# Performance work log

Measured on AMD Instinct MI355X. Metric: run time of the kernel, lower is better.

## Reference

```python
import jax, jax.numpy as jnp
import numpy as np

B, DIM, H, W = 2, 64, 128, 128
D_STATE = 8
D_INNER = int(2.0 * DIM)          # 128
DT_RANK = int(np.ceil(DIM / 16))  # 4
CDBL = DT_RANK + 2 * D_STATE      # 20
HID = 3 * DIM                     # 192 (ffn_expansion_factor=3)
PS = 8                            # EDFFN patch size
EPS = 1e-5


def setup_inputs() -> dict:
    key = jax.random.key(0)
    ks = jax.random.split(key, 20)
    n = lambda k, s, sc=0.02: jax.random.normal(k, s, jnp.float32) * sc
    # dt bias init as in SS2D.dt_init
    rng = np.random.default_rng(0)
    dt = np.exp(rng.uniform(size=D_INNER) * (np.log(0.1) - np.log(0.001)) + np.log(0.001)).clip(min=1e-4)
    dt_b = (dt + np.log(-np.expm1(-dt))).astype(np.float32)
    A_logs = np.log(np.arange(1, D_STATE + 1, dtype=np.float32))[None, :].repeat(D_INNER, 0)
    return {
        "x": jax.random.normal(ks[0], (B, DIM, H, W), jnp.float32),
        "norm1_w": jnp.ones((DIM,), jnp.float32), "norm1_b": jnp.zeros((DIM,), jnp.float32),
        "in_proj_w": n(ks[1], (2 * D_INNER, DIM)),
        "conv2d_w": n(ks[2], (D_INNER, 1, 3, 3), 0.1), "conv2d_b": jnp.zeros((D_INNER,), jnp.float32),
        "x_proj_w": n(ks[3], (CDBL, D_INNER)),
        "x_conv_w": n(ks[4], (CDBL, 1, 7), 0.1), "x_conv_b": jnp.zeros((CDBL,), jnp.float32),
        "dt_w": n(ks[5], (D_INNER, DT_RANK), DT_RANK ** -0.5), "dt_b": jnp.asarray(dt_b),
        "A_logs": jnp.asarray(A_logs), "Ds": jnp.ones((D_INNER,), jnp.float32),
        "out_norm_w": jnp.ones((D_INNER,), jnp.float32), "out_norm_b": jnp.zeros((D_INNER,), jnp.float32),
        "out_proj_w": n(ks[6], (DIM, D_INNER)),
        "norm2_w": jnp.ones((DIM,), jnp.float32), "norm2_b": jnp.zeros((DIM,), jnp.float32),
        "pin_w": n(ks[7], (2 * HID, DIM)),
        "dw_w": n(ks[8], (2 * HID, 1, 3, 3), 0.1),
        "fft_param": jnp.ones((DIM, 1, 1, PS, PS // 2 + 1), jnp.float32),
        "pout_w": n(ks[9], (DIM, HID)),
    }


def _ln_ch(x, w, b):  # LayerNorm over channel dim of BCHW (WithBias_LayerNorm)
    mu = x.mean(1, keepdims=True)
    var = x.var(1, keepdims=True)
    return (x - mu) / jnp.sqrt(var + EPS) * w[None, :, None, None] + b[None, :, None, None]


def _dwconv2d(x, w, b=None):
    y = jax.lax.conv_general_dilated(x, w, (1, 1), [(1, 1), (1, 1)],
                                     dimension_numbers=("NCHW", "OIHW", "NCHW"),
                                     feature_group_count=x.shape[1])
    return y if b is None else y + b[None, :, None, None]


def _dwconv1d(x, w, b):
    y = jax.lax.conv_general_dilated(x, w, (1,), [(3, 3)],
                                     dimension_numbers=("NCH", "OIH", "NCH"),
                                     feature_group_count=x.shape[1])
    return y + b[None, :, None]


def _gelu(x):
    return jax.nn.gelu(x, approximate=False)


def _selective_scan(u, delta, A, Bs, Cs, Ds):
    # u, delta: [B,D,L]; A: [D,N]; Bs, Cs: [B,N,L]; Ds: [D]
    dA = jnp.exp(jnp.einsum("bdl,dn->lbdn", delta, A))          # [L,B,D,N]
    dBu = jnp.einsum("bdl,bnl->lbdn", delta * u, Bs)            # [L,B,D,N]
    Cseq = jnp.transpose(Cs, (2, 0, 1))                         # [L,B,N]

    def step(h, inp):
        dA_l, dBu_l, C_l = inp
        h = dA_l * h + dBu_l
        y = jnp.einsum("bdn,bn->bd", h, C_l)
        return h, y

    h0 = jnp.zeros(dA.shape[1:], dA.dtype)
    _, ys = jax.lax.scan(step, h0, (dA, dBu, Cseq))             # ys: [L,B,D]
    y = jnp.transpose(ys, (1, 2, 0))                            # [B,D,L]
    return y + Ds[None, :, None] * u


def _ss2d(x, in_proj_w, conv2d_w, conv2d_b, x_proj_w, x_conv_w, x_conv_b,
          dt_w, dt_b, A_logs, Ds, out_norm_w, out_norm_b, out_proj_w):
    b, c, h, w = x.shape
    xh = jnp.transpose(x, (0, 2, 3, 1))                          # [B,H,W,C]
    xz = jnp.einsum("bhwc,oc->bhwo", xh, in_proj_w)
    xi, z = jnp.split(xz, 2, axis=-1)
    xi = jnp.transpose(xi, (0, 3, 1, 2))                         # [B,Di,H,W]
    xi = _gelu(_dwconv2d(xi, conv2d_w, conv2d_b))
    L = h * w
    xs = xi.reshape(b, D_INNER, L)
    x_dbl = jnp.einsum("bdl,cd->bcl", xs, x_proj_w)
    x_dbl = _dwconv1d(x_dbl, x_conv_w, x_conv_b)
    dts, Bs, Cs = x_dbl[:, :DT_RANK], x_dbl[:, DT_RANK:DT_RANK + D_STATE], x_dbl[:, DT_RANK + D_STATE:]
    dts = jnp.einsum("brl,dr->bdl", dts, dt_w)
    delta = jax.nn.softplus(dts + dt_b[None, :, None])
    A = -jnp.exp(A_logs)
    y = _selective_scan(xs, delta, A, Bs, Cs, Ds)                # [B,Di,L]
    y = jnp.transpose(y, (0, 2, 1)).reshape(b, h, w, D_INNER)
    mu = y.mean(-1, keepdims=True)
    var = y.var(-1, keepdims=True)
    y = (y - mu) / jnp.sqrt(var + EPS) * out_norm_w + out_norm_b
    y = y * _gelu(z)
    out = jnp.einsum("bhwd,cd->bhwc", y, out_proj_w)
    return jnp.transpose(out, (0, 3, 1, 2))


def _edffn(x, pin_w, dw_w, fft_param, pout_w):
    b, c, h, w = x.shape
    y = jnp.einsum("bchw,oc->bohw", x, pin_w)                    # [B,2*HID,H,W]
    y = _dwconv2d(y, dw_w)
    x1, x2 = jnp.split(y, 2, axis=1)
    y = _gelu(x1) * x2
    y = jnp.einsum("bchw,oc->bohw", y, pout_w)                   # [B,DIM,H,W]
    # per-8x8-patch FFT filtering
    p = y.reshape(b, DIM, h // PS, PS, w // PS, PS).transpose(0, 1, 2, 4, 3, 5)
    pf = jnp.fft.rfft2(p, axes=(-2, -1)) * fft_param
    p = jnp.fft.irfft2(pf, s=(PS, PS), axes=(-2, -1))
    return p.transpose(0, 1, 2, 4, 3, 5).reshape(b, DIM, h, w)


def reference(x, norm1_w, norm1_b, in_proj_w, conv2d_w, conv2d_b, x_proj_w, x_conv_w,
              x_conv_b, dt_w, dt_b, A_logs, Ds, out_norm_w, out_norm_b, out_proj_w,
              norm2_w, norm2_b, pin_w, dw_w, fft_param, pout_w):
    # EVS forward, att=True, idx=3 (odd -> flip H,W)
    x = jnp.flip(x, axis=(-2, -1))
    x = x + _ss2d(_ln_ch(x, norm1_w, norm1_b), in_proj_w, conv2d_w, conv2d_b,
                  x_proj_w, x_conv_w, x_conv_b, dt_w, dt_b, A_logs, Ds,
                  out_norm_w, out_norm_b, out_proj_w)
    x = x + _edffn(_ln_ch(x, norm2_w, norm2_b), pin_w, dw_w, fft_param, pout_w)
    return x
```

## Files before the change

### kernel.cpp

```cpp
#include <hip/hip_runtime.h>
#include <hip/hip_bf16.h>

#define DEV __device__ __forceinline__

constexpr int BATCH = 2;
constexpr int DIM   = 64;
constexpr int HH    = 128, WW = 128;
constexpr int L     = HH * WW;
constexpr int DIN   = 128;
constexpr int DST   = 8;
constexpr int CDBL  = 20;
constexpr int HID   = 192;
constexpr int SEG   = 256;
constexpr int NSEG  = L / SEG;
constexpr int NSEGA = 256;

constexpr long OFF_XF    = 0;
constexpr long OFF_T     = OFF_XF    + (long)BATCH*DIM*L;
constexpr long OFF_XZ    = OFF_T     + (long)BATCH*DIM*L;
constexpr long OFF_XS    = OFF_XZ    + (long)BATCH*2*DIN*L;
constexpr long OFF_DBL   = OFF_XS    + (long)BATCH*DIN*L;
constexpr long OFF_DBL2  = OFF_DBL   + (long)BATCH*CDBL*L;
constexpr long OFF_DELTA = OFF_DBL2  + (long)BATCH*CDBL*L;
constexpr long OFF_Y     = OFF_DELTA + (long)BATCH*DIN*L;
constexpr long OFF_HEND  = OFF_Y     + (long)BATCH*DIN*L;
constexpr long OFF_APROD = OFF_HEND  + (long)BATCH*DIN*NSEGA*DST;
constexpr long OFF_CARRY = OFF_APROD + (long)BATCH*DIN*NSEGA*DST;
constexpr long OFF_H1    = OFF_XS;
constexpr long OFF_YFF   = OFF_H1    + (long)BATCH*2*HID*L;
constexpr long OFF_G     = OFF_CARRY;
constexpr long OFF_AEXP  = OFF_DELTA;

DEV float gelu_f(float x) { return 0.5f * x * (1.0f + erff(x * 0.70710678118654752f)); }
DEV float softplus_f(float x) { return fmaxf(x, 0.f) + log1pf(__expf(-fabsf(x))); }

template<bool FLIPSAVE>
__global__ void ln_ch_k(const float* __restrict__ in, const float* __restrict__ w,
                        const float* __restrict__ bvec, float* __restrict__ outn,
                        float* __restrict__ src_out) {
    int l = blockIdx.x * 256 + threadIdx.x;
    int b = blockIdx.y;
    long base = (long)b * DIM * L;
    int sl = FLIPSAVE ? (L - 1 - l) : l;
    float v[DIM];
    float mu = 0.f;
    #pragma unroll
    for (int c = 0; c < DIM; c++) { v[c] = in[base + (long)c * L + sl]; mu += v[c]; }
    mu *= (1.f / DIM);
    float var = 0.f;
    #pragma unroll
    for (int c = 0; c < DIM; c++) { float d = v[c] - mu; var += d * d; }
    var *= (1.f / DIM);
    float rs = rsqrtf(var + 1e-5f);
    #pragma unroll
    for (int c = 0; c < DIM; c++) {
        long o = base + (long)c * L + l;
        if (FLIPSAVE) src_out[o] = v[c];
        outn[o] = (v[c] - mu) * rs * w[c] + bvec[c];
    }
}

template<int N, int K, int NT, int PIX, int ACT>
__global__ void gemm4(const float* __restrict__ in, long in_bs,
                      const float* __restrict__ Wm,
                      float* __restrict__ out, long out_bs,
                      const float* __restrict__ aux, long aux_bs) {
    static_assert(N % NT == 0, "NT");
    int l = (blockIdx.x * 256 + threadIdx.x) * PIX;
    int b = blockIdx.y;
    int n0 = blockIdx.z * NT;
    const float* Ap = in + (long)b * in_bs + l;
    float acc[NT][PIX];
    #pragma unroll
    for (int i = 0; i < NT; i++)
        #pragma unroll
        for (int p = 0; p < PIX; p++) acc[i][p] = 0.f;
    #pragma unroll 4
    for (int k = 0; k < K; k++) {
        float a[PIX];
        if (PIX == 4) {
            float4 a4 = *(const float4*)(Ap + (long)k * L);
            a[0] = a4.x; a[1] = a4.y; a[2] = a4.z; a[3] = a4.w;
        } else if (PIX == 2) {
            float2 a2 = *(const float2*)(Ap + (long)k * L);
            a[0] = a2.x; a[1] = a2.y;
        } else {
            a[0] = Ap[(long)k * L];
        }
        #pragma unroll
        for (int i = 0; i < NT; i++) {
            float wv = Wm[(long)(n0 + i) * K + k];
            #pragma unroll
            for (int p = 0; p < PIX; p++) acc[i][p] = fmaf(a[p], wv, acc[i][p]);
        }
    }
    #pragma unroll
    for (int i = 0; i < NT; i++) {
        long pos = (long)b * out_bs + (long)(n0 + i) * L + l;
        float r[PIX];
        #pragma unroll
        for (int p = 0; p < PIX; p++) r[p] = acc[i][p];
        if (ACT == 2) {
            const float* rp = aux + (long)b * aux_bs + (long)(n0 + i) * L + l;
            #pragma unroll
            for (int p = 0; p < PIX; p++) r[p] += rp[p];
        }
        if (PIX == 4) {
            float4 st = {r[0], r[1], r[2], r[3]};
            *(float4*)(out + pos) = st;
        } else if (PIX == 2) {
            float2 st = {r[0], r[1]};
            *(float2*)(out + pos) = st;
        } else {
            out[pos] = r[0];
        }
    }
}

__global__ void dwconv3x3_bias_gelu(const float* __restrict__ in, long in_bs,
                                    const float* __restrict__ wgt, const float* __restrict__ bias,
                                    float* __restrict__ out, long out_bs) {
    int l4 = (blockIdx.x * 256 + threadIdx.x) * 4;
    int c = blockIdx.y, b = blockIdx.z;
    int h = l4 >> 7, w = l4 & 127;
    const float* ip = in + (long)b * in_bs + (long)c * L;
    float wv[9];
    #pragma unroll
    for (int i = 0; i < 9; i++) wv[i] = wgt[c * 9 + i];
    float bz = bias[c];
    float acc[4] = {bz, bz, bz, bz};
    #pragma unroll
    for (int kh = 0; kh < 3; kh++) {
        int hh = h + kh - 1;
        if (hh < 0 || hh >= HH) continue;
        const float* row = ip + hh * WW + w;
        float4 m = *(const float4*)row;
        float e[6];
        e[0] = (w > 0) ? row[-1] : 0.f;
        e[1] = m.x; e[2] = m.y; e[3] = m.z; e[4] = m.w;
        e[5] = (w < 124) ? row[4] : 0.f;
        #pragma unroll
        for (int kw = 0; kw < 3; kw++)
            #pragma unroll
            for (int p = 0; p < 4; p++)
                acc[p] = fmaf(wv[kh * 3 + kw], e[kw + p], acc[p]);
    }
    float4 st = {gelu_f(acc[0]), gelu_f(acc[1]), gelu_f(acc[2]), gelu_f(acc[3])};
    *(float4*)(out + (long)b * out_bs + (long)c * L + l4) = st;
}

__global__ void dwconv1d7(const float* __restrict__ in, const float* __restrict__ wgt,
                          const float* __restrict__ bias, float* __restrict__ out) {
    int l = blockIdx.x * 256 + threadIdx.x;
    int c = blockIdx.y, b = blockIdx.z;
    const float* ip = in + ((long)b * CDBL + c) * L;
    float s = bias[c];
    #pragma unroll
    for (int k = 0; k < 7; k++) {
        int p = l + k - 3;
        if (p >= 0 && p < L) s += wgt[c * 7 + k] * ip[p];
    }
    out[((long)b * CDBL + c) * L + l] = s;
}

__global__ void a_prep(const float* __restrict__ A_logs, float* __restrict__ Aexp) {
    int i = blockIdx.x * 256 + threadIdx.x;
    if (i < DIN * DST) Aexp[i] = -__expf(A_logs[i]);
}

__global__ void scan_p1(const float* __restrict__ u, const float* __restrict__ dbl2,
                        const float* __restrict__ Aexp, const float* __restrict__ dtw,
                        const float* __restrict__ dtb,
                        float* __restrict__ hend, float* __restrict__ aprod) {
    int seg = blockIdx.x, b = blockIdx.z;
    int wave = threadIdx.x >> 6, lane = threadIdx.x & 63;
    int d = blockIdx.y * 4 + wave;
    long bd = (long)b * DIN + d;
    int e0 = seg * SEG + lane * 4;
    const float* base = dbl2 + (long)b * CDBL * L + e0;
    float4 r0 = *(const float4*)(base + 0L * L);
    float4 r1 = *(const float4*)(base + 1L * L);
    float4 r2 = *(const float4*)(base + 2L * L);
    float4 r3 = *(const float4*)(base + 3L * L);
    float w0 = dtw[d * 4 + 0], w1 = dtw[d * 4 + 1], w2 = dtw[d * 4 + 2], w3 = dtw[d * 4 + 3];
    float dtbv = dtb[d];
    float dt[4];
    dt[0] = softplus_f(dtbv + w0 * r0.x + w1 * r1.x + w2 * r2.x + w3 * r3.x);
    dt[1] = softplus_f(dtbv + w0 * r0.y + w1 * r1.y + w2 * r2.y + w3 * r3.y);
    dt[2] = softplus_f(dtbv + w0 * r0.z + w1 * r1.z + w2 * r2.z + w3 * r3.z);
    dt[3] = softplus_f(dtbv + w0 * r0.w + w1 * r1.w + w2 * r2.w + w3 * r3.w);
    float4 u4 = *(const float4*)(u + bd * L + e0);
    float du[4] = {dt[0] * u4.x, dt[1] * u4.y, dt[2] * u4.z, dt[3] * u4.w};
    float A[DST], Bb[DST];
    #pragma unroll
    for (int n = 0; n < DST; n++) {
        float an = Aexp[d * DST + n];
        float4 Bn = *(const float4*)(base + (long)(4 + n) * L);
        float a0 = __expf(dt[0] * an), a1 = __expf(dt[1] * an);
        float a2 = __expf(dt[2] * an), a3 = __expf(dt[3] * an);
        float h = du[0] * Bn.x;
        h = fmaf(a1, h, du[1] * Bn.y);
        h = fmaf(a2, h, du[2] * Bn.z);
        h = fmaf(a3, h, du[3] * Bn.w);
        A[n] = a0 * a1 * a2 * a3;
        Bb[n] = h;
    }
    #pragma unroll
    for (int s = 1; s < 64; s <<= 1) {
        #pragma unroll
        for (int n = 0; n < DST; n++) {
            float pa = __shfl_up(A[n], s, 64);
            float pb = __shfl_up(Bb[n], s, 64);
            if (lane >= s) { Bb[n] = fmaf(A[n], pb, Bb[n]); A[n] *= pa; }
        }
    }
    if (lane == 63) {
        #pragma unroll
        for (int n = 0; n < DST; n++) {
            long idx = (bd * DST + n) * NSEG + seg;
            hend[idx] = Bb[n]; aprod[idx] = A[n];
        }
    }
}

__global__ void scan_p2(const float* __restrict__ hend, const float* __restrict__ aprod,
                        float* __restrict__ carryin) {
    int wave = threadIdx.x >> 6, lane = threadIdx.x & 63;
    int chain = blockIdx.x * 4 + wave;
    long idx = (long)chain * NSEG + lane;
    float a = aprod[idx], bv = hend[idx];
    #pragma unroll
    for (int s = 1; s < 64; s <<= 1) {
        float pa = __shfl_up(a, s, 64);
        float pb = __shfl_up(bv, s, 64);
        if (lane >= s) { bv = fmaf(a, pb, bv); a *= pa; }
    }
    float be = __shfl_up(bv, 1, 64);
    carryin[idx] = (lane == 0) ? 0.f : be;
}

__global__ void scan_p3(const float* __restrict__ u, const float* __restrict__ dbl2,
                        const float* __restrict__ Aexp, const float* __restrict__ dtw,
                        const float* __restrict__ dtb, const float* __restrict__ Ds,
                        const float* __restrict__ carryin, float* __restrict__ y) {
    int seg = blockIdx.x, b = blockIdx.z;
    int wave = threadIdx.x >> 6, lane = threadIdx.x & 63;
    int d = blockIdx.y * 4 + wave;
    long bd = (long)b * DIN + d;
    int e0 = seg * SEG + lane * 4;
    const float* base = dbl2 + (long)b * CDBL * L + e0;
    float4 r0 = *(const float4*)(base + 0L * L);
    float4 r1 = *(const float4*)(base + 1L * L);
    float4 r2 = *(const float4*)(base + 2L * L);
    float4 r3 = *(const float4*)(base + 3L * L);
    float w0 = dtw[d * 4 + 0], w1 = dtw[d * 4 + 1], w2 = dtw[d * 4 + 2], w3 = dtw[d * 4 + 3];
    float dtbv = dtb[d];
    float dt[4];
    dt[0] = softplus_f(dtbv + w0 * r0.x + w1 * r1.x + w2 * r2.x + w3 * r3.x);
    dt[1] = softplus_f(dtbv + w0 * r0.y + w1 * r1.y + w2 * r2.y + w3 * r3.y);
    dt[2] = softplus_f(dtbv + w0 * r0.z + w1 * r1.z + w2 * r2.z + w3 * r3.z);
    dt[3] = softplus_f(dtbv + w0 * r0.w + w1 * r1.w + w2 * r2.w + w3 * r3.w);
    float4 u4 = *(const float4*)(u + bd * L + e0);
    float du[4] = {dt[0] * u4.x, dt[1] * u4.y, dt[2] * u4.z, dt[3] * u4.w};
    float A[DST], Bb[DST];
    #pragma unroll
    for (int n = 0; n < DST; n++) {
        float an = Aexp[d * DST + n];
        float4 Bn = *(const float4*)(base + (long)(4 + n) * L);
        float a0 = __expf(dt[0] * an), a1 = __expf(dt[1] * an);
        float a2 = __expf(dt[2] * an), a3 = __expf(dt[3] * an);
        float h = du[0] * Bn.x;
        h = fmaf(a1, h, du[1] * Bn.y);
        h = fmaf(a2, h, du[2] * Bn.z);
        h = fmaf(a3, h, du[3] * Bn.w);
        A[n] = a0 * a1 * a2 * a3;
        Bb[n] = h;
    }
    #pragma unroll
    for (int s = 1; s < 64; s <<= 1) {
        #pragma unroll
        for (int n = 0; n < DST; n++) {
            float pa = __shfl_up(A[n], s, 64);
            float pb = __shfl_up(Bb[n], s, 64);
            if (lane >= s) { Bb[n] = fmaf(A[n], pb, Bb[n]); A[n] *= pa; }
        }
    }
    float Dv = Ds[d];
    float yv[4] = {Dv * u4.x, Dv * u4.y, Dv * u4.z, Dv * u4.w};
    #pragma unroll
    for (int n = 0; n < DST; n++) {
        float carry = carryin[(bd * DST + n) * NSEG + seg];
        float aE = __shfl_up(A[n], 1, 64);
        float bE = __shfl_up(Bb[n], 1, 64);
        if (lane == 0) { aE = 1.f; bE = 0.f; }
        float h = fmaf(aE, carry, bE);
        float an = Aexp[d * DST + n];
        float4 Bn = *(const float4*)(base + (long)(4 + n) * L);
        float4 Cn = *(const float4*)(base + (long)(12 + n) * L);
        h = fmaf(__expf(dt[0] * an), h, du[0] * Bn.x); yv[0] = fmaf(h, Cn.x, yv[0]);
        h = fmaf(__expf(dt[1] * an), h, du[1] * Bn.y); yv[1] = fmaf(h, Cn.y, yv[1]);
        h = fmaf(__expf(dt[2] * an), h, du[2] * Bn.z); yv[2] = fmaf(h, Cn.z, yv[2]);
        h = fmaf(__expf(dt[3] * an), h, du[3] * Bn.w); yv[3] = fmaf(h, Cn.w, yv[3]);
    }
    float4 st = {yv[0], yv[1], yv[2], yv[3]};
    *(float4*)(y + bd * L + e0) = st;
}

__global__ void out_norm_gate(const float* __restrict__ y, const float* __restrict__ xz,
                              const float* __restrict__ w, const float* __restrict__ bb,
                              float* __restrict__ out) {
    __shared__ float sS[4][64], sQ[4][64];
    int wave = threadIdx.x >> 6, lane = threadIdx.x & 63;
    int b = blockIdx.y;
    int p = (blockIdx.x * 2 + (wave >> 1)) * 64 + lane;
    int ch0 = (wave & 1) * 64;
    const float* yp = y + (long)b * DIN * L + (long)ch0 * L + p;
    float v[64];
    float s1 = 0.f, s2 = 0.f;
    #pragma unroll
    for (int c = 0; c < 64; c++) {
        v[c] = yp[(long)c * L];
        s1 += v[c];
        s2 = fmaf(v[c], v[c], s2);
    }
    sS[wave][lane] = s1; sQ[wave][lane] = s2;
    __syncthreads();
    float t1 = s1 + sS[wave ^ 1][lane];
    float t2 = s2 + sQ[wave ^ 1][lane];
    float mu = t1 * (1.f / DIN);
    float var = t2 * (1.f / DIN) - mu * mu;
    float rs = rsqrtf(var + 1e-5f);
    const float* zp = xz + (long)b * 2 * DIN * L + (long)(DIN + ch0) * L + p;
    float* op = out + (long)b * DIN * L + (long)ch0 * L + p;
    #pragma unroll
    for (int c = 0; c < 64; c++) {
        float zz = zp[(long)c * L];
        op[(long)c * L] = ((v[c] - mu) * rs * w[ch0 + c] + bb[ch0 + c]) * gelu_f(zz);
    }
}

__global__ void edffn_conv_gate(const float* __restrict__ in, const float* __restrict__ wgt,
                                float* __restrict__ out) {
    int l4 = (blockIdx.x * 256 + threadIdx.x) * 4;
    int c = blockIdx.y, b = blockIdx.z;
    int h = l4 >> 7, w = l4 & 127;
    const float* i1 = in + ((long)b * 2 * HID + c) * L;
    const float* i2 = i1 + (long)HID * L;
    float w1[9], w2[9];
    #pragma unroll
    for (int i = 0; i < 9; i++) { w1[i] = wgt[c * 9 + i]; w2[i] = wgt[(c + HID) * 9 + i]; }
    float a1[4] = {0.f, 0.f, 0.f, 0.f}, a2[4] = {0.f, 0.f, 0.f, 0.f};
    #pragma unroll
    for (int kh = 0; kh < 3; kh++) {
        int hh = h + kh - 1;
        if (hh < 0 || hh >= HH) continue;
        const float* r1 = i1 + hh * WW + w;
        const float* r2 = i2 + hh * WW + w;
        float4 m1 = *(const float4*)r1;
        float4 m2 = *(const float4*)r2;
        float e1[6], e2[6];
        e1[0] = (w > 0) ? r1[-1] : 0.f;  e2[0] = (w > 0) ? r2[-1] : 0.f;
        e1[1] = m1.x; e1[2] = m1.y; e1[3] = m1.z; e1[4] = m1.w;
        e2[1] = m2.x; e2[2] = m2.y; e2[3] = m2.z; e2[4] = m2.w;
        e1[5] = (w < 124) ? r1[4] : 0.f; e2[5] = (w < 124) ? r2[4] : 0.f;
        #pragma unroll
        for (int kw = 0; kw < 3; kw++)
            #pragma unroll
            for (int p = 0; p < 4; p++) {
                a1[p] = fmaf(w1[kh * 3 + kw], e1[kw + p], a1[p]);
                a2[p] = fmaf(w2[kh * 3 + kw], e2[kw + p], a2[p]);
            }
    }
    float4 st = {gelu_f(a1[0]) * a2[0], gelu_f(a1[1]) * a2[1],
                 gelu_f(a1[2]) * a2[2], gelu_f(a1[3]) * a2[3]};
    *(float4*)(out + ((long)b * HID + c) * L + l4) = st;
}

__global__ void gk_kernel(const float* __restrict__ fp, float* __restrict__ g) {
    int c = blockIdx.x;
    int t = threadIdx.x;
    int a = t >> 3, b2 = t & 7;
    const float PI4 = 0.78539816339744831f;
    float s = 0.f;
    for (int k1 = 0; k1 < 8; k1++) {
        float R = fp[c * 40 + k1 * 5 + 0] + ((b2 & 1) ? -1.f : 1.f) * fp[c * 40 + k1 * 5 + 4];
        for (int k2 = 1; k2 < 4; k2++)
            R += 2.f * fp[c * 40 + k1 * 5 + k2] * cosf(PI4 * (float)(k2 * b2));
        s += cosf(PI4 * (float)(k1 * a)) * R;
    }
    g[c * 64 + t] = s * (1.f / 64.f);
}

__global__ void patch_conv_res(const float* __restrict__ yff, const float* __restrict__ g,
                               const float* __restrict__ res, float* __restrict__ out) {
    int t = blockIdx.x * 256 + threadIdx.x;
    int patch = t >> 3, u = t & 7;
    int c = blockIdx.y, b = blockIdx.z;
    int pi = patch >> 4, pj = patch & 15;
    const float* base = yff + ((long)b * DIM + c) * L + (pi * 8) * WW + pj * 8;
    float4 qa[8], qb[8];
    #pragma unroll
    for (int a = 0; a < 8; a++) {
        int r = (u - a) & 7;
        qa[a] = *(const float4*)(base + r * WW);
        qb[a] = *(const float4*)(base + r * WW + 4);
    }
    float acc[8];
    #pragma unroll
    for (int v = 0; v < 8; v++) acc[v] = 0.f;
    #pragma unroll
    for (int a = 0; a < 8; a++) {
        float q[8] = {qa[a].x, qa[a].y, qa[a].z, qa[a].w,
                      qb[a].x, qb[a].y, qb[a].z, qb[a].w};
        #pragma unroll
        for (int b3 = 0; b3 < 8; b3++) {
            float gv = g[c * 64 + a * 8 + b3];
            #pragma unroll
            for (int v = 0; v < 8; v++)
                acc[v] = fmaf(gv, q[(v - b3) & 7], acc[v]);
        }
    }
    long o = ((long)b * DIM + c) * L + (pi * 8 + u) * WW + pj * 8;
    float4 r0 = *(const float4*)(res + o);
    float4 r1 = *(const float4*)(res + o + 4);
    float4 s0 = {acc[0] + r0.x, acc[1] + r0.y, acc[2] + r0.z, acc[3] + r0.w};
    float4 s1 = {acc[4] + r1.x, acc[5] + r1.y, acc[6] + r1.z, acc[7] + r1.w};
    *(float4*)(out + o) = s0;
    *(float4*)(out + o + 4) = s1;
}

extern "C" void kernel_launch(void* const* d_in, const int* in_sizes, int n_in,
                              void* d_out, int out_size, void* d_ws, size_t ws_size,
                              hipStream_t stream) {
    const float* x         = (const float*)d_in[0];
    const float* norm1_w   = (const float*)d_in[1];
    const float* norm1_b   = (const float*)d_in[2];
    const float* in_proj_w = (const float*)d_in[3];
    const float* conv2d_w  = (const float*)d_in[4];
    const float* conv2d_b  = (const float*)d_in[5];
    const float* x_proj_w  = (const float*)d_in[6];
    const float* x_conv_w  = (const float*)d_in[7];
    const float* x_conv_b  = (const float*)d_in[8];
    const float* dt_w      = (const float*)d_in[9];
    const float* dt_b      = (const float*)d_in[10];
    const float* A_logs    = (const float*)d_in[11];
    const float* Ds        = (const float*)d_in[12];
    const float* out_norm_w= (const float*)d_in[13];
    const float* out_norm_b= (const float*)d_in[14];
    const float* out_proj_w= (const float*)d_in[15];
    const float* norm2_w   = (const float*)d_in[16];
    const float* norm2_b   = (const float*)d_in[17];
    const float* pin_w     = (const float*)d_in[18];
    const float* dw_w      = (const float*)d_in[19];
    const float* fft_param = (const float*)d_in[20];
    const float* pout_w    = (const float*)d_in[21];
    float* ws  = (float*)d_ws;
    float* out = (float*)d_out;

    dim3 blk(256);
    const int GX  = L / 256;
    const int GX4 = L / (256 * 4);
    const int GX2 = L / (256 * 2);

    a_prep<<<dim3(4), blk, 0, stream>>>(A_logs, ws + OFF_AEXP);
    ln_ch_k<true><<<dim3(GX, BATCH), blk, 0, stream>>>(x, norm1_w, norm1_b, ws + OFF_T, ws + OFF_XF);
    gemm4<256, 64, 16, 4, 0><<<dim3(GX4, BATCH, 16), blk, 0, stream>>>(
        ws + OFF_T, (long)DIM * L, in_proj_w, ws + OFF_XZ, (long)2 * DIN * L, nullptr, 0);
    dwconv3x3_bias_gelu<<<dim3(GX4, DIN, BATCH), blk, 0, stream>>>(
        ws + OFF_XZ, (long)2 * DIN * L, conv2d_w, conv2d_b, ws + OFF_XS, (long)DIN * L);
    gemm4<20, 128, 5, 2, 0><<<dim3(GX2, BATCH, 4), blk, 0, stream>>>(
        ws + OFF_XS, (long)DIN * L, x_proj_w, ws + OFF_DBL, (long)CDBL * L, nullptr, 0);
    dwconv1d7<<<dim3(GX, CDBL, BATCH), blk, 0, stream>>>(ws + OFF_DBL, x_conv_w, x_conv_b, ws + OFF_DBL2);
    scan_p1<<<dim3(NSEG, DIN / 4, BATCH), blk, 0, stream>>>(
        ws + OFF_XS, ws + OFF_DBL2, ws + OFF_AEXP, dt_w, dt_b, ws + OFF_HEND, ws + OFF_APROD);
    scan_p2<<<dim3(BATCH * DIN * DST / 4), blk, 0, stream>>>(
        ws + OFF_HEND, ws + OFF_APROD, ws + OFF_CARRY);
    scan_p3<<<dim3(NSEG, DIN / 4, BATCH), blk, 0, stream>>>(
        ws + OFF_XS, ws + OFF_DBL2, ws + OFF_AEXP, dt_w, dt_b, Ds, ws + OFF_CARRY, ws + OFF_Y);
    out_norm_gate<<<dim3(L / 128, BATCH), blk, 0, stream>>>(ws + OFF_Y, ws + OFF_XZ,
                                                            out_norm_w, out_norm_b, ws + OFF_DELTA);
    gemm4<64, 128, 8, 4, 2><<<dim3(GX4, BATCH, 8), blk, 0, stream>>>(
        ws + OFF_DELTA, (long)DIN * L, out_proj_w, ws + OFF_XF, (long)DIM * L,
        ws + OFF_XF, (long)DIM * L);
    ln_ch_k<false><<<dim3(GX, BATCH), blk, 0, stream>>>(ws + OFF_XF, norm2_w, norm2_b,
                                                        ws + OFF_T, nullptr);
    gemm4<384, 64, 16, 4, 0><<<dim3(GX4, BATCH, 24), blk, 0, stream>>>(
        ws + OFF_T, (long)DIM * L, pin_w, ws + OFF_H1, (long)2 * HID * L, nullptr, 0);
    edffn_conv_gate<<<dim3(GX4, HID, BATCH), blk, 0, stream>>>(ws + OFF_H1, dw_w, ws + OFF_XZ);
    gemm4<64, 192, 8, 4, 0><<<dim3(GX4, BATCH, 8), blk, 0, stream>>>(
        ws + OFF_XZ, (long)HID * L, pout_w, ws + OFF_YFF, (long)DIM * L, nullptr, 0);
    gk_kernel<<<dim3(DIM), dim3(64), 0, stream>>>(fft_param, ws + OFF_G);
    patch_conv_res<<<dim3(8, DIM, BATCH), blk, 0, stream>>>(ws + OFF_YFF, ws + OFF_G,
                                                            ws + OFF_XF, out);
}
```

Measured before the change: 289.2 us.

## Restructure selective scan into local pass plus cumulative-dt carry fix and fold small kernels

The chunked scan changes shape. The first pass now also computes the local output with zero carry and writes the prefix sum of dt per position. A light fix-up kernel then adds each segment's carry contribution as exp(A*cumdt)*carry*C, so the recurrence no longer has to be recomputed in a third pass. The a_prep and gk_kernel kernels are folded into their consumers, and the 1D conv is vectorised to four outputs per thread. This saves launches and redundant exp and scan work, but adds a cumdt buffer write and read, and relies on exp(A*cumdt) staying numerically accurate.

Result: faster. 257.1 us (-11.1%).

```diff
diff --git a/kernel.cpp b/kernel.cpp
--- a/kernel.cpp
+++ b/kernel.cpp
@@ -28,8 +28,7 @@
 constexpr long OFF_CARRY = OFF_APROD + (long)BATCH*DIN*NSEGA*DST;
 constexpr long OFF_H1    = OFF_XS;
 constexpr long OFF_YFF   = OFF_H1    + (long)BATCH*2*HID*L;
-constexpr long OFF_G     = OFF_CARRY;
-constexpr long OFF_AEXP  = OFF_DELTA;
+constexpr long OFF_CDT   = OFF_DELTA;
 
 DEV float gelu_f(float x) { return 0.5f * x * (1.0f + erff(x * 0.70710678118654752f)); }
 DEV float softplus_f(float x) { return fmaxf(x, 0.f) + log1pf(__expf(-fabsf(x))); }
@@ -151,27 +150,37 @@
 
 __global__ void dwconv1d7(const float* __restrict__ in, const float* __restrict__ wgt,
                           const float* __restrict__ bias, float* __restrict__ out) {
-    int l = blockIdx.x * 256 + threadIdx.x;
+    int l4 = (blockIdx.x * 256 + threadIdx.x) * 4;
     int c = blockIdx.y, b = blockIdx.z;
     const float* ip = in + ((long)b * CDBL + c) * L;
-    float s = bias[c];
-    #pragma unroll
-    for (int k = 0; k < 7; k++) {
-        int p = l + k - 3;
-        if (p >= 0 && p < L) s += wgt[c * 7 + k] * ip[p];
-    }
-    out[((long)b * CDBL + c) * L + l] = s;
-}
-
-__global__ void a_prep(const float* __restrict__ A_logs, float* __restrict__ Aexp) {
-    int i = blockIdx.x * 256 + threadIdx.x;
-    if (i < DIN * DST) Aexp[i] = -__expf(A_logs[i]);
-}
-
-__global__ void scan_p1(const float* __restrict__ u, const float* __restrict__ dbl2,
-                        const float* __restrict__ Aexp, const float* __restrict__ dtw,
-                        const float* __restrict__ dtb,
-                        float* __restrict__ hend, float* __restrict__ aprod) {
+    float wv[7];
+    #pragma unroll
+    for (int k = 0; k < 7; k++) wv[k] = wgt[c * 7 + k];
+    float bz = bias[c];
+    float e[10];
+    float4 m = *(const float4*)(ip + l4);
+    e[0] = (l4 >= 3) ? ip[l4 - 3] : 0.f;
+    e[1] = (l4 >= 2) ? ip[l4 - 2] : 0.f;
+    e[2] = (l4 >= 1) ? ip[l4 - 1] : 0.f;
+    e[3] = m.x; e[4] = m.y; e[5] = m.z; e[6] = m.w;
+    e[7] = (l4 + 4 < L) ? ip[l4 + 4] : 0.f;
+    e[8] = (l4 + 5 < L) ? ip[l4 + 5] : 0.f;
+    e[9] = (l4 + 6 < L) ? ip[l4 + 6] : 0.f;
+    float acc[4] = {bz, bz, bz, bz};
+    #pragma unroll
+    for (int k = 0; k < 7; k++)
+        #pragma unroll
+        for (int p = 0; p < 4; p++)
+            acc[p] = fmaf(wv[k], e[p + k], acc[p]);
+    float4 st = {acc[0], acc[1], acc[2], acc[3]};
+    *(float4*)(out + ((long)b * CDBL + c) * L + l4) = st;
+}
+
+__global__ void scan_p1y(const float* __restrict__ u, const float* __restrict__ dbl2,
+                         const float* __restrict__ A_logs, const float* __restrict__ dtw,
+                         const float* __restrict__ dtb, const float* __restrict__ Ds,
+                         float* __restrict__ y0, float* __restrict__ cdt_out,
+                         float* __restrict__ hend, float* __restrict__ aprod) {
     int seg = blockIdx.x, b = blockIdx.z;
     int wave = threadIdx.x >> 6, lane = threadIdx.x & 63;
     int d = blockIdx.y * 4 + wave;
@@ -189,12 +198,25 @@
     dt[1] = softplus_f(dtbv + w0 * r0.y + w1 * r1.y + w2 * r2.y + w3 * r3.y);
     dt[2] = softplus_f(dtbv + w0 * r0.z + w1 * r1.z + w2 * r2.z + w3 * r3.z);
     dt[3] = softplus_f(dtbv + w0 * r0.w + w1 * r1.w + w2 * r2.w + w3 * r3.w);
+    float c0 = dt[0], c1 = c0 + dt[1], c2 = c1 + dt[2], c3 = c2 + dt[3];
+    float S = c3;
+    #pragma unroll
+    for (int s = 1; s < 64; s <<= 1) {
+        float pv = __shfl_up(S, s, 64);
+        if (lane >= s) S += pv;
+    }
+    float Sex = S - c3;
+    float4 cd = {c0 + Sex, c1 + Sex, c2 + Sex, c3 + Sex};
+    *(float4*)(cdt_out + bd * L + e0) = cd;
     float4 u4 = *(const float4*)(u + bd * L + e0);
     float du[4] = {dt[0] * u4.x, dt[1] * u4.y, dt[2] * u4.z, dt[3] * u4.w};
+    float Aexp[DST];
+    #pragma unroll
+    for (int n = 0; n < DST; n++) Aexp[n] = -__expf(A_logs[d * DST + n]);
     float A[DST], Bb[DST];
     #pragma unroll
     for (int n = 0; n < DST; n++) {
-        float an = Aexp[d * DST + n];
+        float an = Aexp[n];
         float4 Bn = *(const float4*)(base + (long)(4 + n) * L);
         float a0 = __expf(dt[0] * an), a1 = __expf(dt[1] * an);
         float a2 = __expf(dt[2] * an), a3 = __expf(dt[3] * an);
@@ -221,6 +243,23 @@
             hend[idx] = Bb[n]; aprod[idx] = A[n];
         }
     }
+    float Dv = Ds[d];
+    float yv[4] = {Dv * u4.x, Dv * u4.y, Dv * u4.z, Dv * u4.w};
+    #pragma unroll
+    for (int n = 0; n < DST; n++) {
+        float bE = __shfl_up(Bb[n], 1, 64);
+        if (lane == 0) bE = 0.f;
+        float h = bE;
+        float an = Aexp[n];
+        float4 Bn = *(const float4*)(base + (long)(4 + n) * L);
+        float4 Cn = *(const float4*)(base + (long)(12 + n) * L);
+        h = fmaf(__expf(dt[0] * an), h, du[0] * Bn.x); yv[0] = fmaf(h, Cn.x, yv[0]);
+        h = fmaf(__expf(dt[1] * an), h, du[1] * Bn.y); yv[1] = fmaf(h, Cn.y, yv[1]);
+        h = fmaf(__expf(dt[2] * an), h, du[2] * Bn.z); yv[2] = fmaf(h, Cn.z, yv[2]);
+        h = fmaf(__expf(dt[3] * an), h, du[3] * Bn.w); yv[3] = fmaf(h, Cn.w, yv[3]);
+    }
+    float4 st = {yv[0], yv[1], yv[2], yv[3]};
+    *(float4*)(y0 + bd * L + e0) = st;
 }
 
 __global__ void scan_p2(const float* __restrict__ hend, const float* __restrict__ aprod,
@@ -239,71 +278,28 @@
     carryin[idx] = (lane == 0) ? 0.f : be;
 }
 
-__global__ void scan_p3(const float* __restrict__ u, const float* __restrict__ dbl2,
-                        const float* __restrict__ Aexp, const float* __restrict__ dtw,
-                        const float* __restrict__ dtb, const float* __restrict__ Ds,
-                        const float* __restrict__ carryin, float* __restrict__ y) {
+__global__ void scan_fix(const float* __restrict__ A_logs, const float* __restrict__ dbl2,
+                         const float* __restrict__ cdt, const float* __restrict__ carryin,
+                         float* __restrict__ y) {
     int seg = blockIdx.x, b = blockIdx.z;
     int wave = threadIdx.x >> 6, lane = threadIdx.x & 63;
     int d = blockIdx.y * 4 + wave;
     long bd = (long)b * DIN + d;
     int e0 = seg * SEG + lane * 4;
-    const float* base = dbl2 + (long)b * CDBL * L + e0;
-    float4 r0 = *(const float4*)(base + 0L * L);
-    float4 r1 = *(const float4*)(base + 1L * L);
-    float4 r2 = *(const float4*)(base + 2L * L);
-    float4 r3 = *(const float4*)(base + 3L * L);
-    float w0 = dtw[d * 4 + 0], w1 = dtw[d * 4 + 1], w2 = dtw[d * 4 + 2], w3 = dtw[d * 4 + 3];
-    float dtbv = dtb[d];
-    float dt[4];
-    dt[0] = softplus_f(dtbv + w0 * r0.x + w1 * r1.x + w2 * r2.x + w3 * r3.x);
-    dt[1] = softplus_f(dtbv + w0 * r0.y + w1 * r1.y + w2 * r2.y + w3 * r3.y);
-    dt[2] = softplus_f(dtbv + w0 * r0.z + w1 * r1.z + w2 * r2.z + w3 * r3.z);
-    dt[3] = softplus_f(dtbv + w0 * r0.w + w1 * r1.w + w2 * r2.w + w3 * r3.w);
-    float4 u4 = *(const float4*)(u + bd * L + e0);
-    float du[4] = {dt[0] * u4.x, dt[1] * u4.y, dt[2] * u4.z, dt[3] * u4.w};
-    float A[DST], Bb[DST];
-    #pragma unroll
-    for (int n = 0; n < DST; n++) {
-        float an = Aexp[d * DST + n];
-        float4 Bn = *(const float4*)(base + (long)(4 + n) * L);
-        float a0 = __expf(dt[0] * an), a1 = __expf(dt[1] * an);
-        float a2 = __expf(dt[2] * an), a3 = __expf(dt[3] * an);
-        float h = du[0] * Bn.x;
-        h = fmaf(a1, h, du[1] * Bn.y);
-        h = fmaf(a2, h, du[2] * Bn.z);
-        h = fmaf(a3, h, du[3] * Bn.w);
-        A[n] = a0 * a1 * a2 * a3;
-        Bb[n] = h;
-    }
-    #pragma unroll
-    for (int s = 1; s < 64; s <<= 1) {
-        #pragma unroll
-        for (int n = 0; n < DST; n++) {
-            float pa = __shfl_up(A[n], s, 64);
-            float pb = __shfl_up(Bb[n], s, 64);
-            if (lane >= s) { Bb[n] = fmaf(A[n], pb, Bb[n]); A[n] *= pa; }
-        }
-    }
-    float Dv = Ds[d];
-    float yv[4] = {Dv * u4.x, Dv * u4.y, Dv * u4.z, Dv * u4.w};
+    float4 cd = *(const float4*)(cdt + bd * L + e0);
+    float4 yv = *(const float4*)(y + bd * L + e0);
+    const float* cbase = dbl2 + (long)b * CDBL * L + 12L * L + e0;
     #pragma unroll
     for (int n = 0; n < DST; n++) {
         float carry = carryin[(bd * DST + n) * NSEG + seg];
-        float aE = __shfl_up(A[n], 1, 64);
-        float bE = __shfl_up(Bb[n], 1, 64);
-        if (lane == 0) { aE = 1.f; bE = 0.f; }
-        float h = fmaf(aE, carry, bE);
-        float an = Aexp[d * DST + n];
-        float4 Bn = *(const float4*)(base + (long)(4 + n) * L);
-        float4 Cn = *(const float4*)(base + (long)(12 + n) * L);
-        h = fmaf(__expf(dt[0] * an), h, du[0] * Bn.x); yv[0] = fmaf(h, Cn.x, yv[0]);
-        h = fmaf(__expf(dt[1] * an), h, du[1] * Bn.y); yv[1] = fmaf(h, Cn.y, yv[1]);
-        h = fmaf(__expf(dt[2] * an), h, du[2] * Bn.z); yv[2] = fmaf(h, Cn.z, yv[2]);
-        h = fmaf(__expf(dt[3] * an), h, du[3] * Bn.w); yv[3] = fmaf(h, Cn.w, yv[3]);
-    }
-    float4 st = {yv[0], yv[1], yv[2], yv[3]};
-    *(float4*)(y + bd * L + e0) = st;
+        float an = -__expf(A_logs[d * DST + n]);
+        float4 Cn = *(const float4*)(cbase + (long)n * L);
+        yv.x = fmaf(__expf(an * cd.x) * carry, Cn.x, yv.x);
+        yv.y = fmaf(__expf(an * cd.y) * carry, Cn.y, yv.y);
+        yv.z = fmaf(__expf(an * cd.z) * carry, Cn.z, yv.z);
+        yv.w = fmaf(__expf(an * cd.w) * carry, Cn.w, yv.w);
+    }
+    *(float4*)(y + bd * L + e0) = yv;
 }
 
 __global__ void out_norm_gate(const float* __restrict__ y, const float* __restrict__ xz,
@@ -376,26 +372,28 @@
     *(float4*)(out + ((long)b * HID + c) * L + l4) = st;
 }
 
-__global__ void gk_kernel(const float* __restrict__ fp, float* __restrict__ g) {
-    int c = blockIdx.x;
-    int t = threadIdx.x;
-    int a = t >> 3, b2 = t & 7;
+__global__ void patch_conv_res(const float* __restrict__ yff, const float* __restrict__ fp,
+                               const float* __restrict__ res, float* __restrict__ out) {
+    __shared__ float ct[8];
+    __shared__ float gs[64];
+    int c = blockIdx.y, b = blockIdx.z;
     const float PI4 = 0.78539816339744831f;
-    float s = 0.f;
-    for (int k1 = 0; k1 < 8; k1++) {
-        float R = fp[c * 40 + k1 * 5 + 0] + ((b2 & 1) ? -1.f : 1.f) * fp[c * 40 + k1 * 5 + 4];
-        for (int k2 = 1; k2 < 4; k2++)
-            R += 2.f * fp[c * 40 + k1 * 5 + k2] * cosf(PI4 * (float)(k2 * b2));
-        s += cosf(PI4 * (float)(k1 * a)) * R;
-    }
-    g[c * 64 + t] = s * (1.f / 64.f);
-}
-
-__global__ void patch_conv_res(const float* __restrict__ yff, const float* __restrict__ g,
-                               const float* __restrict__ res, float* __restrict__ out) {
+    if (threadIdx.x < 8) ct[threadIdx.x] = cosf(PI4 * (float)threadIdx.x);
+    __syncthreads();
+    if (threadIdx.x < 64) {
+        int a = threadIdx.x >> 3, b2 = threadIdx.x & 7;
+        float s = 0.f;
+        for (int k1 = 0; k1 < 8; k1++) {
+            float R = fp[c * 40 + k1 * 5 + 0] + ((b2 & 1) ? -1.f : 1.f) * fp[c * 40 + k1 * 5 + 4];
+            for (int k2 = 1; k2 < 4; k2++)
+                R += 2.f * fp[c * 40 + k1 * 5 + k2] * ct[(k2 * b2) & 7];
+            s += ct[(k1 * a) & 7] * R;
+        }
+        gs[threadIdx.x] = s * (1.f / 64.f);
+    }
+    __syncthreads();
     int t = blockIdx.x * 256 + threadIdx.x;
     int patch = t >> 3, u = t & 7;
-    int c = blockIdx.y, b = blockIdx.z;
     int pi = patch >> 4, pj = patch & 15;
     const float* base = yff + ((long)b * DIM + c) * L + (pi * 8) * WW + pj * 8;
     float4 qa[8], qb[8];
@@ -414,7 +412,7 @@
                       qb[a].x, qb[a].y, qb[a].z, qb[a].w};
         #pragma unroll
         for (int b3 = 0; b3 < 8; b3++) {
-            float gv = g[c * 64 + a * 8 + b3];
+            float gv = gs[a * 8 + b3];
             #pragma unroll
             for (int v = 0; v < 8; v++)
                 acc[v] = fmaf(gv, q[(v - b3) & 7], acc[v]);
@@ -462,7 +460,6 @@
     const int GX4 = L / (256 * 4);
     const int GX2 = L / (256 * 2);
 
-    a_prep<<<dim3(4), blk, 0, stream>>>(A_logs, ws + OFF_AEXP);
     ln_ch_k<true><<<dim3(GX, BATCH), blk, 0, stream>>>(x, norm1_w, norm1_b, ws + OFF_T, ws + OFF_XF);
     gemm4<256, 64, 16, 4, 0><<<dim3(GX4, BATCH, 16), blk, 0, stream>>>(
         ws + OFF_T, (long)DIM * L, in_proj_w, ws + OFF_XZ, (long)2 * DIN * L, nullptr, 0);
@@ -470,13 +467,14 @@
         ws + OFF_XZ, (long)2 * DIN * L, conv2d_w, conv2d_b, ws + OFF_XS, (long)DIN * L);
     gemm4<20, 128, 5, 2, 0><<<dim3(GX2, BATCH, 4), blk, 0, stream>>>(
         ws + OFF_XS, (long)DIN * L, x_proj_w, ws + OFF_DBL, (long)CDBL * L, nullptr, 0);
-    dwconv1d7<<<dim3(GX, CDBL, BATCH), blk, 0, stream>>>(ws + OFF_DBL, x_conv_w, x_conv_b, ws + OFF_DBL2);
-    scan_p1<<<dim3(NSEG, DIN / 4, BATCH), blk, 0, stream>>>(
-        ws + OFF_XS, ws + OFF_DBL2, ws + OFF_AEXP, dt_w, dt_b, ws + OFF_HEND, ws + OFF_APROD);
+    dwconv1d7<<<dim3(GX4, CDBL, BATCH), blk, 0, stream>>>(ws + OFF_DBL, x_conv_w, x_conv_b, ws + OFF_DBL2);
+    scan_p1y<<<dim3(NSEG, DIN / 4, BATCH), blk, 0, stream>>>(
+        ws + OFF_XS, ws + OFF_DBL2, A_logs, dt_w, dt_b, Ds,
+        ws + OFF_Y, ws + OFF_CDT, ws + OFF_HEND, ws + OFF_APROD);
     scan_p2<<<dim3(BATCH * DIN * DST / 4), blk, 0, stream>>>(
         ws + OFF_HEND, ws + OFF_APROD, ws + OFF_CARRY);
-    scan_p3<<<dim3(NSEG, DIN / 4, BATCH), blk, 0, stream>>>(
-        ws + OFF_XS, ws + OFF_DBL2, ws + OFF_AEXP, dt_w, dt_b, Ds, ws + OFF_CARRY, ws + OFF_Y);
+    scan_fix<<<dim3(NSEG, DIN / 4, BATCH), blk, 0, stream>>>(
+        A_logs, ws + OFF_DBL2, ws + OFF_CDT, ws + OFF_CARRY, ws + OFF_Y);
     out_norm_gate<<<dim3(L / 128, BATCH), blk, 0, stream>>>(ws + OFF_Y, ws + OFF_XZ,
                                                             out_norm_w, out_norm_b, ws + OFF_DELTA);
     gemm4<64, 128, 8, 4, 2><<<dim3(GX4, BATCH, 8), blk, 0, stream>>>(
@@ -489,7 +487,6 @@
     edffn_conv_gate<<<dim3(GX4, HID, BATCH), blk, 0, stream>>>(ws + OFF_H1, dw_w, ws + OFF_XZ);
     gemm4<64, 192, 8, 4, 0><<<dim3(GX4, BATCH, 8), blk, 0, stream>>>(
         ws + OFF_XZ, (long)HID * L, pout_w, ws + OFF_YFF, (long)DIM * L, nullptr, 0);
-    gk_kernel<<<dim3(DIM), dim3(64), 0, stream>>>(fft_param, ws + OFF_G);
-    patch_conv_res<<<dim3(8, DIM, BATCH), blk, 0, stream>>>(ws + OFF_YFF, ws + OFF_G,
+    patch_conv_res<<<dim3(8, DIM, BATCH), blk, 0, stream>>>(ws + OFF_YFF, fft_param,
                                                             ws + OFF_XF, out);
 }
```
